# Kernel tuning notes

Hardware: AMD Instinct MI355X
Metric: run time of the kernel (lower is better)

The kernel has to match this reference:

```python
import jax, jax.numpy as jnp
import numpy as np

B, L, A, D = 4, 512, 8, 256
H = 256  # hidden_dim
O = 256  # output_dim


def setup_inputs() -> dict:
    key = jax.random.key(0)
    ks = jax.random.split(key, 12)
    s = 0.05
    return {
        "x": jax.random.normal(ks[0], (B, L, A, D), dtype=jnp.float32),
        "conv_w": jax.random.normal(ks[1], (H, D), dtype=jnp.float32) * s,
        "conv_b": jax.random.normal(ks[2], (H,), dtype=jnp.float32) * s,
        "theta_w": jax.random.normal(ks[3], (H, H), dtype=jnp.float32) * s,
        "theta_b": jax.random.normal(ks[4], (H,), dtype=jnp.float32) * s,
        "phi_w": jax.random.normal(ks[5], (H, H), dtype=jnp.float32) * s,
        "phi_b": jax.random.normal(ks[6], (H,), dtype=jnp.float32) * s,
        "g_w": jax.random.normal(ks[7], (H, H), dtype=jnp.float32) * s,
        "g_b": jax.random.normal(ks[8], (H,), dtype=jnp.float32) * s,
        "f_w": jax.random.normal(ks[9], (O, H), dtype=jnp.float32) * s,
        "f_b": jax.random.normal(ks[10], (O,), dtype=jnp.float32) * s,
    }


def reference(x, conv_w, conv_b, theta_w, theta_b, phi_w, phi_b, g_w, g_b, f_w, f_b):
    batch, length, n_agents, _ = x.shape
    # residual: identity (input_dim == output_dim, stride 1)
    res = x
    # conv with kernel (1,1): pointwise projection over channel dim
    h = jnp.einsum('blad,hd->blah', x, conv_w) + conv_b  # [B,L,A,H]
    N = length * n_agents
    h = h.reshape(batch, N, H)
    theta = jnp.einsum('bnh,kh->bnk', h, theta_w) + theta_b  # [B,N,H]
    phi = jnp.einsum('bnh,kh->bnk', h, phi_w) + phi_b        # [B,N,H]
    g = jnp.einsum('bnh,kh->bnk', h, g_w) + g_b              # [B,N,H]
    scores = jnp.einsum('bnk,bmk->bnm', theta, phi) / jnp.sqrt(jnp.asarray(H, theta.dtype))
    y = jax.nn.softmax(scores, axis=2)                       # [B,N,N]
    z = jnp.einsum('bnm,bmk->bnk', y, g) / jnp.sqrt(jnp.asarray(N, y.dtype))
    out = jnp.einsum('bnk,ok->bno', z, f_w) + f_b            # [B,N,O]
    out = out.reshape(batch, length, n_agents, O)
    return out + res
```

## Files before the change

### kernel.cpp

```cpp
#include <hip/hip_runtime.h>

typedef unsigned short u16;
typedef __bf16 bf16x8 __attribute__((ext_vector_type(8)));
typedef float f32x4 __attribute__((ext_vector_type(4)));
typedef float f32x16 __attribute__((ext_vector_type(16)));
typedef float float4v __attribute__((ext_vector_type(4)));
typedef unsigned short u16x8 __attribute__((ext_vector_type(8)));
typedef unsigned short u16x4 __attribute__((ext_vector_type(4)));

#define MFMA16(a, b, c) __builtin_amdgcn_mfma_f32_16x16x32_bf16(a, b, c, 0, 0, 0)
#define MFMA32(a, b, c) __builtin_amdgcn_mfma_f32_32x32x16_bf16(a, b, c, 0, 0, 0)

__device__ __forceinline__ u16 f2bf(float f) {
  union { float f; unsigned u; } v; v.f = f;
  unsigned r = v.u + 0x7fffu + ((v.u >> 16) & 1u);
  return (u16)(r >> 16);
}

__device__ __forceinline__ void gload16(const void* g, void* l) {
  __builtin_amdgcn_global_load_lds(
      (__attribute__((address_space(1))) void*)g,
      (__attribute__((address_space(3))) void*)l, 16, 0, 0);
}

__device__ __forceinline__ unsigned cvtpk(float lo, float hi) {
  unsigned r;
  asm("v_cvt_pk_bf16_f32 %0, %1, %2" : "=v"(r) : "v"(lo), "v"(hi));
  return r;
}
__device__ __forceinline__ void plswap(unsigned& a, unsigned& b) {
  asm volatile("v_permlane32_swap_b32 %0, %1" : "+v"(a), "+v"(b));
}

__global__ __launch_bounds__(256) void convert_k(
    const float* __restrict__ x, const float* __restrict__ cw,
    const float* __restrict__ tw, const float* __restrict__ pw,
    const float* __restrict__ gw, const float* __restrict__ fw,
    const float* __restrict__ tb, const float* __restrict__ pb,
    const float* __restrict__ gb,
    u16* __restrict__ xb, u16* __restrict__ cwb, u16* __restrict__ wcat,
    u16* __restrict__ fwb, float* __restrict__ bcat) {
  const int idx = blockIdx.x * 256 + threadIdx.x;
  const float* src;
  u16* dst;
  int off;
  if (idx < 1048576)      { src = x;  dst = xb;            off = idx; }
  else if (idx < 1064960) { src = cw; dst = cwb;           off = idx - 1048576; }
  else if (idx < 1081344) { src = tw; dst = wcat;          off = idx - 1064960; }
  else if (idx < 1097728) { src = pw; dst = wcat + 65536;  off = idx - 1081344; }
  else if (idx < 1114112) { src = gw; dst = wcat + 131072; off = idx - 1097728; }
  else if (idx < 1130496) { src = fw; dst = fwb;           off = idx - 1114112; }
  else if (idx < 1130688) {
    int j = (idx - 1130496) * 4;
#pragma unroll
    for (int i = 0; i < 4; ++i) {
      int k = j + i;
      bcat[k] = (k < 256) ? tb[k] : (k < 512) ? pb[k - 256] : gb[k - 512];
    }
    return;
  } else return;
  float4v v = *(const float4v*)(src + (size_t)off * 4);
  u16x4 o;
#pragma unroll
  for (int i = 0; i < 4; ++i) o[i] = f2bf(v[i]);
  *(u16x4*)(dst + (size_t)off * 4) = o;
}

template <int OM>
__global__ __launch_bounds__(256) void gemm_bt(
    const u16* __restrict__ A, const u16* __restrict__ W,
    const float* __restrict__ bias, void* __restrict__ Cout,
    const float* __restrict__ res, int K, int ldc) {
  __shared__ u16 As[8192];
  __shared__ u16 Bs[8192];
  const int t = threadIdx.x;
  const int lane = t & 63, w = t >> 6;
  const int brow = blockIdx.x * 128, bcol = blockIdx.y * 128;
  const int wr = (w >> 1) * 64, wc = (w & 1) * 64;
  f32x4 acc[4][4];
#pragma unroll
  for (int i = 0; i < 4; ++i)
#pragma unroll
    for (int j = 0; j < 4; ++j)
#pragma unroll
      for (int r = 0; r < 4; ++r) acc[i][j][r] = 0.0f;

  const int sr = t >> 3, sc8 = (t & 7) * 8;
  const u16* gA = A + (size_t)(brow + sr) * K + sc8;
  const u16* gW = W + (size_t)(bcol + sr) * K + sc8;

  for (int kt = 0; kt < K; kt += 64) {
#pragma unroll
    for (int c = 0; c < 4; ++c) {
      gload16(gA + (size_t)c * 32 * K + kt, &As[c * 2048 + t * 8]);
      gload16(gW + (size_t)c * 32 * K + kt, &Bs[c * 2048 + t * 8]);
    }
    __syncthreads();
#pragma unroll
    for (int kk = 0; kk < 2; ++kk) {
      const int ko = kk * 32 + (lane >> 4) * 8;
      bf16x8 af[4], bfr[4];
#pragma unroll
      for (int i = 0; i < 4; ++i)
        af[i] = *(const bf16x8*)(&As[(wr + i * 16 + (lane & 15)) * 64 + ko]);
#pragma unroll
      for (int j = 0; j < 4; ++j)
        bfr[j] = *(const bf16x8*)(&Bs[(wc + j * 16 + (lane & 15)) * 64 + ko]);
#pragma unroll
      for (int i = 0; i < 4; ++i)
#pragma unroll
        for (int j = 0; j < 4; ++j)
          acc[i][j] = MFMA16(af[i], bfr[j], acc[i][j]);
    }
    __syncthreads();
  }

  const int r0 = (lane >> 4) * 4, c0 = lane & 15;
#pragma unroll
  for (int i = 0; i < 4; ++i)
#pragma unroll
    for (int j = 0; j < 4; ++j) {
      const int col = bcol + wc + j * 16 + c0;
      const float bv = bias[col];
#pragma unroll
      for (int r = 0; r < 4; ++r) {
        const size_t o = (size_t)(brow + wr + i * 16 + r0 + r) * ldc + col;
        if (OM == 0) ((u16*)Cout)[o] = f2bf(acc[i][j][r] + bv);
        else         ((float*)Cout)[o] = acc[i][j][r] + bv + res[o];
      }
    }
}

__global__ __launch_bounds__(256) void transpose_g_k(
    const u16* __restrict__ tpg, u16* __restrict__ gT) {
  __shared__ u16 T[64][65];
  const int t = threadIdx.x;
  const int bm = (blockIdx.x & 63) * 64;
  const int bk = ((blockIdx.x >> 6) & 3) * 64;
  const int b = blockIdx.x >> 8;
  const int r = t >> 3, c8 = (t & 7) * 8;
#pragma unroll
  for (int ch = 0; ch < 2; ++ch) {
    u16x8 v = *(const u16x8*)(tpg + (size_t)(b * 4096 + bm + r + ch * 32) * 768 + 512 + bk + c8);
#pragma unroll
    for (int j = 0; j < 8; ++j) T[r + ch * 32][c8 + j] = v[j];
  }
  __syncthreads();
#pragma unroll
  for (int ch = 0; ch < 2; ++ch) {
    u16x8 o;
#pragma unroll
    for (int j = 0; j < 8; ++j) o[j] = T[c8 + j][r + ch * 32];
    *(u16x8*)(gT + (size_t)(b * 256 + bk + r + ch * 32) * 4096 + bm + c8) = o;
  }
}

__global__ __launch_bounds__(256, 2) void flash2(
    const u16* __restrict__ tpg, const u16* __restrict__ gT,
    u16* __restrict__ Zp, float* __restrict__ Lp) {
  __shared__ u16 Kl[2][32 * 256];
  __shared__ u16 Vl[2][256 * 32];

  const int t = threadIdx.x;
  const int lane = t & 63, w = t >> 6;
  const int l31 = lane & 31, hi = lane >> 5;
  const int bid = blockIdx.x;
  const int b = bid >> 7;
  const int quarter = (bid >> 5) & 3;
  const int qt = bid & 31;
  const int q0 = qt * 128 + w * 32;
  const int kv0 = quarter * 1024;

  bf16x8 q[16];
  {
    const u16* qp = tpg + (size_t)(b * 4096 + q0 + l31) * 768 + hi * 8;
#pragma unroll
    for (int ks = 0; ks < 16; ++ks) q[ks] = *(const bf16x8*)(qp + ks * 16);
  }

  f32x16 zacc[8];
#pragma unroll
  for (int i = 0; i < 8; ++i)
#pragma unroll
    for (int j = 0; j < 16; ++j) zacc[i][j] = 0.0f;
  float ell = 0.0f;

  const int ksr = t >> 5, ksc = t & 31;

  auto stage = [&](int tile, int bi) {
    const size_t krow0 = (size_t)(b * 4096 + kv0 + tile * 32);
#pragma unroll
    for (int ch = 0; ch < 4; ++ch) {
      int r = ch * 8 + ksr;
      gload16(tpg + (krow0 + r) * 768 + 256 + ((ksc ^ r) * 8), &Kl[bi][ch * 2048 + t * 8]);
    }
#pragma unroll
    for (int ch = 0; ch < 4; ++ch) {
      int u = ch * 256 + t;
      int r = u >> 2, c16 = u & 3;
      gload16(gT + (size_t)(b * 256 + r) * 4096 + kv0 + tile * 32 + ((c16 ^ ((r >> 1) & 3)) * 8),
              &Vl[bi][u * 8]);
    }
  };

  stage(0, 0);
  __syncthreads();

  for (int tile = 0; tile < 32; ++tile) {
    const int cur = tile & 1;
    if (tile + 1 < 32) stage(tile + 1, cur ^ 1);

    f32x16 s;
#pragma unroll
    for (int j = 0; j < 16; ++j) s[j] = 0.0f;
    const u16* kb = &Kl[cur][0];
#pragma unroll
    for (int ks = 0; ks < 16; ++ks) {
      bf16x8 kf = *(const bf16x8*)(kb + l31 * 256 + (((2 * ks + hi) ^ l31) * 8));
      s = MFMA32(kf, q[ks], s);
    }

    bf16x8 pa[2];
#pragma unroll
    for (int half = 0; half < 2; ++half) {
      float p[8];
#pragma unroll
      for (int g = 0; g < 8; ++g) {
        p[g] = __builtin_amdgcn_exp2f(s[half * 8 + g] * 0.09016844f);
        ell += p[g];
      }
      unsigned x0 = cvtpk(p[0], p[1]), y0 = cvtpk(p[4], p[5]);
      unsigned x1 = cvtpk(p[2], p[3]), y1 = cvtpk(p[6], p[7]);
      plswap(x0, y0);
      plswap(x1, y1);
      union { unsigned u[4]; bf16x8 v; } cc;
      cc.u[0] = x0; cc.u[1] = x1; cc.u[2] = y0; cc.u[3] = y1;
      pa[half] = cc.v;
    }

    const u16* vb = &Vl[cur][0];
#pragma unroll
    for (int ks2 = 0; ks2 < 2; ++ks2) {
#pragma unroll
      for (int nt = 0; nt < 8; ++nt) {
        int row = nt * 32 + l31;
        bf16x8 vv = *(const bf16x8*)(vb + row * 32 + (((2 * ks2 + hi) ^ ((row >> 1) & 3)) * 8));
        zacc[nt] = MFMA32(pa[ks2], vv, zacc[nt]);
      }
    }
    __syncthreads();
  }

  ell += __shfl_xor(ell, 32, 64);

#pragma unroll
  for (int g = 0; g < 16; ++g) {
    int r = (g & 3) + 8 * (g >> 2) + 4 * hi;
    size_t rowoff = ((size_t)(quarter * 16384 + b * 4096 + q0 + r)) * 256 + l31;
#pragma unroll
    for (int nt = 0; nt < 8; ++nt) Zp[rowoff + nt * 32] = f2bf(zacc[nt][g]);
  }
  if (lane < 32) Lp[quarter * 16384 + b * 4096 + q0 + l31] = ell;
}

__global__ __launch_bounds__(256) void merge2(
    const u16* __restrict__ Zp, const float* __restrict__ Lp, u16* __restrict__ zb) {
  const int idx = blockIdx.x * 256 + threadIdx.x;
  const int m = idx >> 5;
  const int c = (idx & 31) * 8;
  const float l = Lp[m] + Lp[16384 + m] + Lp[32768 + m] + Lp[49152 + m];
  const float inv = 1.0f / (l * 64.0f);
  float acc[8];
#pragma unroll
  for (int j = 0; j < 8; ++j) acc[j] = 0.0f;
#pragma unroll
  for (int qd = 0; qd < 4; ++qd) {
    u16x8 v = *(const u16x8*)(Zp + ((size_t)(qd * 16384) + m) * 256 + c);
#pragma unroll
    for (int j = 0; j < 8; ++j) {
      union { unsigned u; float f; } cv;
      cv.u = ((unsigned)v[j]) << 16;
      acc[j] += cv.f;
    }
  }
  u16x8 o;
#pragma unroll
  for (int j = 0; j < 8; ++j) o[j] = f2bf(acc[j] * inv);
  *(u16x8*)(zb + (size_t)m * 256 + c) = o;
}

extern "C" void kernel_launch(void* const* d_in, const int* in_sizes, int n_in,
                              void* d_out, int out_size, void* d_ws, size_t ws_size,
                              hipStream_t stream) {
  const float* x  = (const float*)d_in[0];
  const float* cw = (const float*)d_in[1];
  const float* cb = (const float*)d_in[2];
  const float* tw = (const float*)d_in[3];
  const float* tb = (const float*)d_in[4];
  const float* pw = (const float*)d_in[5];
  const float* pb = (const float*)d_in[6];
  const float* gw = (const float*)d_in[7];
  const float* gb = (const float*)d_in[8];
  const float* fw = (const float*)d_in[9];
  const float* fb = (const float*)d_in[10];

  char* ws = (char*)d_ws;
  u16*   tpg  = (u16*)(ws);
  u16*   gT   = (u16*)(ws + 25165824);
  u16*   zb   = (u16*)(ws + 25165824);
  u16*   xb   = (u16*)(ws + 33554432);
  u16*   hb   = (u16*)(ws + 41943040);
  u16*   Zp   = (u16*)(ws + 33554432);
  u16*   cwb  = (u16*)(ws + 67239936);
  u16*   wcat = (u16*)(ws + 67371008);
  u16*   fwb  = (u16*)(ws + 67764224);
  float* bcat = (float*)(ws + 67895296);
  float* Lp   = (float*)d_out;

  convert_k<<<4417, 256, 0, stream>>>(x, cw, tw, pw, gw, fw, tb, pb, gb,
                                      xb, cwb, wcat, fwb, bcat);
  gemm_bt<0><<<dim3(128, 2), 256, 0, stream>>>(xb, cwb, cb, (void*)hb, nullptr, 256, 256);
  gemm_bt<0><<<dim3(128, 6), 256, 0, stream>>>(hb, wcat, bcat, (void*)tpg, nullptr, 256, 768);
  transpose_g_k<<<1024, 256, 0, stream>>>(tpg, gT);
  flash2<<<512, 256, 0, stream>>>(tpg, gT, Zp, Lp);
  merge2<<<2048, 256, 0, stream>>>(Zp, Lp, zb);
  gemm_bt<1><<<dim3(128, 2), 256, 0, stream>>>(zb, fwb, fb, d_out, x, 256, 256);
}
```

Measured before the change: 215.2 us.

## Fuse x conversion into first GEMM and split-K merge into output GEMM

The bf16 conversion of x moves into the first projection GEMM, which now loads fp32 rows and packs them into LDS, so the separate convert pass and its xb buffer go away. The flash partial merge (sum of four quarter partials and normalisation) moves into the output GEMM's A-tile loading, removing the merge2 kernel and the zb round trip. The softmax denominators are now stored as bf16, which loses some precision, and s_setprio is added around the MFMA loops in flash2. Because the output GEMM runs with two column blocks, it reads the Zp partials twice.

After: 215.9 us. About the same (+0.3%).

```diff
diff --git a/kernel.cpp b/kernel.cpp
--- a/kernel.cpp
+++ b/kernel.cpp
@@ -16,6 +16,10 @@
   unsigned r = v.u + 0x7fffu + ((v.u >> 16) & 1u);
   return (u16)(r >> 16);
 }
+__device__ __forceinline__ float bf2f(u16 b) {
+  union { unsigned u; float f; } v; v.u = ((unsigned)b) << 16;
+  return v.f;
+}
 
 __device__ __forceinline__ void gload16(const void* g, void* l) {
   __builtin_amdgcn_global_load_lds(
@@ -32,26 +36,25 @@
   asm volatile("v_permlane32_swap_b32 %0, %1" : "+v"(a), "+v"(b));
 }
 
-__global__ __launch_bounds__(256) void convert_k(
-    const float* __restrict__ x, const float* __restrict__ cw,
+__global__ __launch_bounds__(256) void convert_w(
+    const float* __restrict__ cw,
     const float* __restrict__ tw, const float* __restrict__ pw,
     const float* __restrict__ gw, const float* __restrict__ fw,
     const float* __restrict__ tb, const float* __restrict__ pb,
     const float* __restrict__ gb,
-    u16* __restrict__ xb, u16* __restrict__ cwb, u16* __restrict__ wcat,
-    u16* __restrict__ fwb, float* __restrict__ bcat) {
+    u16* __restrict__ cwb, u16* __restrict__ wcat, u16* __restrict__ fwb,
+    float* __restrict__ bcat) {
   const int idx = blockIdx.x * 256 + threadIdx.x;
   const float* src;
   u16* dst;
   int off;
-  if (idx < 1048576)      { src = x;  dst = xb;            off = idx; }
-  else if (idx < 1064960) { src = cw; dst = cwb;           off = idx - 1048576; }
-  else if (idx < 1081344) { src = tw; dst = wcat;          off = idx - 1064960; }
-  else if (idx < 1097728) { src = pw; dst = wcat + 65536;  off = idx - 1081344; }
-  else if (idx < 1114112) { src = gw; dst = wcat + 131072; off = idx - 1097728; }
-  else if (idx < 1130496) { src = fw; dst = fwb;           off = idx - 1114112; }
-  else if (idx < 1130688) {
-    int j = (idx - 1130496) * 4;
+  if (idx < 16384)      { src = cw; dst = cwb;  off = idx; }
+  else if (idx < 32768) { src = tw; dst = wcat; off = idx - 16384; }
+  else if (idx < 49152) { src = pw; dst = wcat + 65536;  off = idx - 32768; }
+  else if (idx < 65536) { src = gw; dst = wcat + 131072; off = idx - 49152; }
+  else if (idx < 81920) { src = fw; dst = fwb;  off = idx - 65536; }
+  else if (idx < 82112) {
+    int j = (idx - 81920) * 4;
 #pragma unroll
     for (int i = 0; i < 4; ++i) {
       int k = j + i;
@@ -66,11 +69,9 @@
   *(u16x4*)(dst + (size_t)off * 4) = o;
 }
 
-template <int OM>
 __global__ __launch_bounds__(256) void gemm_bt(
     const u16* __restrict__ A, const u16* __restrict__ W,
-    const float* __restrict__ bias, void* __restrict__ Cout,
-    const float* __restrict__ res, int K, int ldc) {
+    const float* __restrict__ bias, u16* __restrict__ Cout, int K, int ldc) {
   __shared__ u16 As[8192];
   __shared__ u16 Bs[8192];
   const int t = threadIdx.x;
@@ -125,8 +126,84 @@
 #pragma unroll
       for (int r = 0; r < 4; ++r) {
         const size_t o = (size_t)(brow + wr + i * 16 + r0 + r) * ldc + col;
-        if (OM == 0) ((u16*)Cout)[o] = f2bf(acc[i][j][r] + bv);
-        else         ((float*)Cout)[o] = acc[i][j][r] + bv + res[o];
+        Cout[o] = f2bf(acc[i][j][r] + bv);
+      }
+    }
+}
+
+__global__ __launch_bounds__(256) void gemm_h(
+    const float* __restrict__ X, const u16* __restrict__ W,
+    const float* __restrict__ bias, u16* __restrict__ Cout) {
+  __shared__ u16 As[8192];
+  __shared__ u16 Bs[8192];
+  const int t = threadIdx.x;
+  const int lane = t & 63, w = t >> 6;
+  const int brow = blockIdx.x * 128, bcol = blockIdx.y * 128;
+  const int wr = (w >> 1) * 64, wc = (w & 1) * 64;
+  f32x4 acc[4][4];
+#pragma unroll
+  for (int i = 0; i < 4; ++i)
+#pragma unroll
+    for (int j = 0; j < 4; ++j)
+#pragma unroll
+      for (int r = 0; r < 4; ++r) acc[i][j][r] = 0.0f;
+
+  const int sr = t >> 3, sc8 = (t & 7) * 8;
+  const u16* gW = W + (size_t)(bcol + sr) * 256 + sc8;
+  const int ar = t & 127, ach = t >> 7;
+  const float* gX = X + (size_t)(brow + ar) * 256 + ach * 32;
+
+  for (int kt = 0; kt < 256; kt += 64) {
+#pragma unroll
+    for (int c = 0; c < 4; ++c)
+      gload16(gW + (size_t)c * 32 * 256 + kt, &Bs[c * 2048 + t * 8]);
+    u16x8 pk[4];
+#pragma unroll
+    for (int j = 0; j < 4; ++j) {
+      float4v v0 = *(const float4v*)(gX + kt + j * 8);
+      float4v v1 = *(const float4v*)(gX + kt + j * 8 + 4);
+#pragma unroll
+      for (int e = 0; e < 4; ++e) { pk[j][e] = f2bf(v0[e]); pk[j][4 + e] = f2bf(v1[e]); }
+    }
+#pragma unroll
+    for (int j = 0; j < 4; ++j) {
+      int unit = (ach * 4 + j) ^ (ar & 7);
+      *(u16x8*)(&As[ar * 64 + unit * 8]) = pk[j];
+    }
+    __syncthreads();
+#pragma unroll
+    for (int kk = 0; kk < 2; ++kk) {
+      const int ko = kk * 32 + (lane >> 4) * 8;
+      bf16x8 af[4], bfr[4];
+#pragma unroll
+      for (int i = 0; i < 4; ++i) {
+        int R = wr + i * 16 + (lane & 15);
+        int unit = (kk * 4 + (lane >> 4)) ^ (R & 7);
+        af[i] = *(const bf16x8*)(&As[R * 64 + unit * 8]);
+      }
+#pragma unroll
+      for (int j = 0; j < 4; ++j)
+        bfr[j] = *(const bf16x8*)(&Bs[(wc + j * 16 + (lane & 15)) * 64 + ko]);
+#pragma unroll
+      for (int i = 0; i < 4; ++i)
+#pragma unroll
+        for (int j = 0; j < 4; ++j)
+          acc[i][j] = MFMA16(af[i], bfr[j], acc[i][j]);
+    }
+    __syncthreads();
+  }
+
+  const int r0 = (lane >> 4) * 4, c0 = lane & 15;
+#pragma unroll
+  for (int i = 0; i < 4; ++i)
+#pragma unroll
+    for (int j = 0; j < 4; ++j) {
+      const int col = bcol + wc + j * 16 + c0;
+      const float bv = bias[col];
+#pragma unroll
+      for (int r = 0; r < 4; ++r) {
+        const size_t o = (size_t)(brow + wr + i * 16 + r0 + r) * 256 + col;
+        Cout[o] = f2bf(acc[i][j][r] + bv);
       }
     }
 }
@@ -157,7 +234,7 @@
 
 __global__ __launch_bounds__(256, 2) void flash2(
     const u16* __restrict__ tpg, const u16* __restrict__ gT,
-    u16* __restrict__ Zp, float* __restrict__ Lp) {
+    u16* __restrict__ Zp, u16* __restrict__ Lpb) {
   __shared__ u16 Kl[2][32 * 256];
   __shared__ u16 Vl[2][256 * 32];
 
@@ -214,11 +291,13 @@
 #pragma unroll
     for (int j = 0; j < 16; ++j) s[j] = 0.0f;
     const u16* kb = &Kl[cur][0];
+    __builtin_amdgcn_s_setprio(1);
 #pragma unroll
     for (int ks = 0; ks < 16; ++ks) {
       bf16x8 kf = *(const bf16x8*)(kb + l31 * 256 + (((2 * ks + hi) ^ l31) * 8));
       s = MFMA32(kf, q[ks], s);
     }
+    __builtin_amdgcn_s_setprio(0);
 
     bf16x8 pa[2];
 #pragma unroll
@@ -239,6 +318,7 @@
     }
 
     const u16* vb = &Vl[cur][0];
+    __builtin_amdgcn_s_setprio(1);
 #pragma unroll
     for (int ks2 = 0; ks2 < 2; ++ks2) {
 #pragma unroll
@@ -248,6 +328,7 @@
         zacc[nt] = MFMA32(pa[ks2], vv, zacc[nt]);
       }
     }
+    __builtin_amdgcn_s_setprio(0);
     __syncthreads();
   }
 
@@ -260,33 +341,97 @@
 #pragma unroll
     for (int nt = 0; nt < 8; ++nt) Zp[rowoff + nt * 32] = f2bf(zacc[nt][g]);
   }
-  if (lane < 32) Lp[quarter * 16384 + b * 4096 + q0 + l31] = ell;
-}
-
-__global__ __launch_bounds__(256) void merge2(
-    const u16* __restrict__ Zp, const float* __restrict__ Lp, u16* __restrict__ zb) {
-  const int idx = blockIdx.x * 256 + threadIdx.x;
-  const int m = idx >> 5;
-  const int c = (idx & 31) * 8;
-  const float l = Lp[m] + Lp[16384 + m] + Lp[32768 + m] + Lp[49152 + m];
-  const float inv = 1.0f / (l * 64.0f);
-  float acc[8];
-#pragma unroll
-  for (int j = 0; j < 8; ++j) acc[j] = 0.0f;
-#pragma unroll
-  for (int qd = 0; qd < 4; ++qd) {
-    u16x8 v = *(const u16x8*)(Zp + ((size_t)(qd * 16384) + m) * 256 + c);
-#pragma unroll
-    for (int j = 0; j < 8; ++j) {
-      union { unsigned u; float f; } cv;
-      cv.u = ((unsigned)v[j]) << 16;
-      acc[j] += cv.f;
-    }
-  }
-  u16x8 o;
-#pragma unroll
-  for (int j = 0; j < 8; ++j) o[j] = f2bf(acc[j] * inv);
-  *(u16x8*)(zb + (size_t)m * 256 + c) = o;
+  if (lane < 32) Lpb[quarter * 16384 + b * 4096 + q0 + l31] = f2bf(ell);
+}
+
+__global__ __launch_bounds__(256) void gemm_out(
+    const u16* __restrict__ Zp, const u16* __restrict__ Lpb,
+    const u16* __restrict__ W, const float* __restrict__ bias,
+    float* __restrict__ Cout, const float* __restrict__ res) {
+  __shared__ u16 As[8192];
+  __shared__ u16 Bs[8192];
+  const int t = threadIdx.x;
+  const int lane = t & 63, w = t >> 6;
+  const int brow = blockIdx.x * 128, bcol = blockIdx.y * 128;
+  const int wr = (w >> 1) * 64, wc = (w & 1) * 64;
+  f32x4 acc[4][4];
+#pragma unroll
+  for (int i = 0; i < 4; ++i)
+#pragma unroll
+    for (int j = 0; j < 4; ++j)
+#pragma unroll
+      for (int r = 0; r < 4; ++r) acc[i][j][r] = 0.0f;
+
+  const int sr = t >> 3, sc8 = (t & 7) * 8;
+  const u16* gW = W + (size_t)(bcol + sr) * 256 + sc8;
+  const int ar = t >> 1, ach = t & 1;
+  const int am = brow + ar;
+  const float linv = 1.0f /
+      ((bf2f(Lpb[am]) + bf2f(Lpb[16384 + am]) + bf2f(Lpb[32768 + am]) + bf2f(Lpb[49152 + am])) *
+       64.0f);
+
+  for (int kt = 0; kt < 256; kt += 64) {
+#pragma unroll
+    for (int c = 0; c < 4; ++c)
+      gload16(gW + (size_t)c * 32 * 256 + kt, &Bs[c * 2048 + t * 8]);
+    const int col0 = kt + ach * 32;
+    float sacc[32];
+#pragma unroll
+    for (int e = 0; e < 32; ++e) sacc[e] = 0.0f;
+#pragma unroll
+    for (int qd = 0; qd < 4; ++qd) {
+      const u16* zp = Zp + ((size_t)(qd * 16384) + am) * 256 + col0;
+#pragma unroll
+      for (int j = 0; j < 4; ++j) {
+        u16x8 v = *(const u16x8*)(zp + j * 8);
+#pragma unroll
+        for (int e = 0; e < 8; ++e) sacc[j * 8 + e] += bf2f(v[e]);
+      }
+    }
+#pragma unroll
+    for (int j = 0; j < 4; ++j) {
+      u16x8 pk;
+#pragma unroll
+      for (int e = 0; e < 8; ++e) pk[e] = f2bf(sacc[j * 8 + e] * linv);
+      int unit = (ach * 4 + j) ^ (ar & 7);
+      *(u16x8*)(&As[ar * 64 + unit * 8]) = pk;
+    }
+    __syncthreads();
+#pragma unroll
+    for (int kk = 0; kk < 2; ++kk) {
+      const int ko = kk * 32 + (lane >> 4) * 8;
+      bf16x8 af[4], bfr[4];
+#pragma unroll
+      for (int i = 0; i < 4; ++i) {
+        int R = wr + i * 16 + (lane & 15);
+        int unit = (kk * 4 + (lane >> 4)) ^ (R & 7);
+        af[i] = *(const bf16x8*)(&As[R * 64 + unit * 8]);
+      }
+#pragma unroll
+      for (int j = 0; j < 4; ++j)
+        bfr[j] = *(const bf16x8*)(&Bs[(wc + j * 16 + (lane & 15)) * 64 + ko]);
+#pragma unroll
+      for (int i = 0; i < 4; ++i)
+#pragma unroll
+        for (int j = 0; j < 4; ++j)
+          acc[i][j] = MFMA16(af[i], bfr[j], acc[i][j]);
+    }
+    __syncthreads();
+  }
+
+  const int r0 = (lane >> 4) * 4, c0 = lane & 15;
+#pragma unroll
+  for (int i = 0; i < 4; ++i)
+#pragma unroll
+    for (int j = 0; j < 4; ++j) {
+      const int col = bcol + wc + j * 16 + c0;
+      const float bv = bias[col];
+#pragma unroll
+      for (int r = 0; r < 4; ++r) {
+        const size_t o = (size_t)(brow + wr + i * 16 + r0 + r) * 256 + col;
+        Cout[o] = acc[i][j][r] + bv + res[o];
+      }
+    }
 }
 
 extern "C" void kernel_launch(void* const* d_in, const int* in_sizes, int n_in,
@@ -307,22 +452,19 @@
   char* ws = (char*)d_ws;
   u16*   tpg  = (u16*)(ws);
   u16*   gT   = (u16*)(ws + 25165824);
-  u16*   zb   = (u16*)(ws + 25165824);
-  u16*   xb   = (u16*)(ws + 33554432);
   u16*   hb   = (u16*)(ws + 41943040);
   u16*   Zp   = (u16*)(ws + 33554432);
+  u16*   Lpb  = (u16*)(ws + 67108864);
   u16*   cwb  = (u16*)(ws + 67239936);
   u16*   wcat = (u16*)(ws + 67371008);
   u16*   fwb  = (u16*)(ws + 67764224);
   float* bcat = (float*)(ws + 67895296);
-  float* Lp   = (float*)d_out;
-
-  convert_k<<<4417, 256, 0, stream>>>(x, cw, tw, pw, gw, fw, tb, pb, gb,
-                                      xb, cwb, wcat, fwb, bcat);
-  gemm_bt<0><<<dim3(128, 2), 256, 0, stream>>>(xb, cwb, cb, (void*)hb, nullptr, 256, 256);
-  gemm_bt<0><<<dim3(128, 6), 256, 0, stream>>>(hb, wcat, bcat, (void*)tpg, nullptr, 256, 768);
+
+  convert_w<<<321, 256, 0, stream>>>(cw, tw, pw, gw, fw, tb, pb, gb,
+                                     cwb, wcat, fwb, bcat);
+  gemm_h<<<dim3(128, 2), 256, 0, stream>>>(x, cwb, cb, hb);
+  gemm_bt<<<dim3(128, 6), 256, 0, stream>>>(hb, wcat, bcat, tpg, 256, 768);
   transpose_g_k<<<1024, 256, 0, stream>>>(tpg, gT);
-  flash2<<<512, 256, 0, stream>>>(tpg, gT, Zp, Lp);
-  merge2<<<2048, 256, 0, stream>>>(Zp, Lp, zb);
-  gemm_bt<1><<<dim3(128, 2), 256, 0, stream>>>(zb, fwb, fb, d_out, x, 256, 256);
-}
+  flash2<<<512, 256, 0, stream>>>(tpg, gT, Zp, Lpb);
+  gemm_out<<<dim3(128, 2), 256, 0, stream>>>(Zp, Lpb, fwb, fb, (float*)d_out, x);
+}
```
